# Optimization experiments

Hardware: AMD Instinct MI355X
Metric: run time of the kernel (lower is better)

The kernel has to match this reference:

```python
import jax, jax.numpy as jnp
import numpy as np

B, L, H = 32, 2048, 512
EPS = 1e-6


def setup_inputs() -> dict:
    key = jax.random.key(0)
    k1, k2 = jax.random.split(key)
    hidden = jax.random.normal(k1, (B, L, H), dtype=jnp.float32)
    # nn.Linear(H, H): weight [H, H], bias [H]; use kaiming-uniform-like scale
    bound = 1.0 / np.sqrt(H)
    W = jax.random.uniform(k2, (H, H), dtype=jnp.float32, minval=-bound, maxval=bound)
    b = jnp.zeros((H,), dtype=jnp.float32)
    return {"hidden": hidden, "W": W, "b": b}


def reference(hidden, W, b):
    Bn, Ln, Hn = hidden.shape

    def step(M, k):
        # k: [B, H]; key == value == hidden[:, t, :]
        v_pred = jnp.einsum("bij,bj->bi", M, k)               # M @ k
        denom = jnp.sum(k * k, axis=-1, keepdims=True) + EPS   # [B, 1]
        delta_v = k - v_pred / denom                           # v - v_pred/denom (v == k)
        M = M + jnp.einsum("bi,bj->bij", delta_v, k)           # outer-product update
        return M, None

    M0 = jnp.zeros((Bn, Hn, Hn), dtype=hidden.dtype)
    xs = jnp.swapaxes(hidden[:, :-1, :], 0, 1)  # [L-1, B, H]
    M, _ = jax.lax.scan(step, M0, xs)

    query = hidden[:, -1, :]                                   # [B, H]
    context = jnp.einsum("bij,bj->bi", M, query)               # [B, H]
    return context @ W.T + b                                   # read_proj
```

## Files before the change

kernel.cpp:

```cpp
#include <hip/hip_runtime.h>
#include <hip/hip_fp16.h>

#define B_  32
#define L_  2048
#define H_  512
#define T_  2047
#define CA  32
#define NC  64
#define EPSF 1e-6f

template <int CTRL>
__device__ __forceinline__ float dpp_shift_add(float x) {
  int t = __builtin_amdgcn_update_dpp(0, __float_as_int(x), CTRL, 0xf, 0xf, true);
  return x + __int_as_float(t);
}
__device__ __forceinline__ float wave_reduce_lane63(float x) {
  x = dpp_shift_add<0x111>(x);
  x = dpp_shift_add<0x112>(x);
  x = dpp_shift_add<0x114>(x);
  x = dpp_shift_add<0x118>(x);
  x = dpp_shift_add<0x142>(x);
  x = dpp_shift_add<0x143>(x);
  return x;
}
__device__ __forceinline__ float rdlane(float v, int l) {
  return __int_as_float(__builtin_amdgcn_readlane(__float_as_int(v), l));
}

__device__ __forceinline__ void load_lds16(const float* g, float* l) {
  __builtin_amdgcn_global_load_lds(
      (const __attribute__((address_space(1))) unsigned int*)(g),
      (__attribute__((address_space(3))) unsigned int*)(l), 16, 0, 0);
}
__device__ __forceinline__ void load_lds16h(const unsigned short* g, unsigned short* l) {
  __builtin_amdgcn_global_load_lds(
      (const __attribute__((address_space(1))) unsigned int*)(g),
      (__attribute__((address_space(3))) unsigned int*)(l), 16, 0, 0);
}

__global__ __launch_bounds__(256) void
deltarule_gram(const float* __restrict__ hidden,
               float* __restrict__ tmT, float* __restrict__ dvec,
               unsigned short* __restrict__ Kh,
               unsigned short* __restrict__ KhT) {
  const int cb = blockIdx.x, b = blockIdx.y;
  const int tid = threadIdx.x, lane = tid & 63, wv = tid >> 6;
  __shared__ __align__(16) float Kc[CA * H_];
  __shared__ float G[CA * 33];

  const float* kb = hidden + ((size_t)b * L_ + (size_t)cb * CA) * H_;
#pragma unroll
  for (int u = 0; u < 16; ++u) {
    const int off = (u * 4 + wv) * 256;
    load_lds16(kb + off + 4 * lane, &Kc[off]);
  }
  __asm__ volatile("s_waitcnt vmcnt(0)" ::: "memory");
  __syncthreads();
  if (cb == NC - 1) {
    if (tid < 128) *(float4*)&Kc[31 * H_ + 4 * tid] = make_float4(0.f, 0.f, 0.f, 0.f);
    __syncthreads();
  }

  if (Kh) {
    unsigned int* dst = (unsigned int*)(Kh + ((size_t)b * L_ + (size_t)cb * CA) * H_);
#pragma unroll
    for (int u = 0; u < 32; ++u) {
      const int i = u * 256 + tid;
      float2 v = *(const float2*)&Kc[2 * i];
      __half2 h2 = __floats2half2_rn(v.x, v.y);
      dst[i] = *(const unsigned int*)&h2;
      *(float2*)&Kc[2 * i] = __half22float2(h2);
    }
    __syncthreads();
  }
  if (KhT) {
    unsigned short* base = KhT + ((size_t)b * NC + cb) * (4 * H_ * 8);
#pragma unroll
    for (int r = 0; r < 2; ++r) {
      const int hh = r * 256 + tid;
#pragma unroll
      for (int g = 0; g < 4; ++g) {
        __half2 h2[4];
#pragma unroll
        for (int e = 0; e < 4; ++e) {
          float a  = Kc[(8 * g + 2 * e) * H_ + hh];
          float b2 = Kc[(8 * g + 2 * e + 1) * H_ + hh];
          h2[e] = __floats2half2_rn(a, b2);
        }
        *(uint4*)(base + (size_t)g * (H_ * 8) + (size_t)hh * 8) = *(const uint4*)h2;
      }
    }
  }

  float kr[8][8];
#pragma unroll
  for (int i = 0; i < 8; ++i) {
    const int r = 8 * wv + i;
    *(float4*)&kr[i][0] = *(const float4*)&Kc[r * H_ + 4 * lane];
    *(float4*)&kr[i][4] = *(const float4*)&Kc[r * H_ + 256 + 4 * lane];
  }
  float g[8] = {0.f, 0.f, 0.f, 0.f, 0.f, 0.f, 0.f, 0.f};
  for (int j = 8 * wv; j < CA; ++j) {
    float kj[8];
    *(float4*)&kj[0] = *(const float4*)&Kc[j * H_ + 4 * lane];
    *(float4*)&kj[4] = *(const float4*)&Kc[j * H_ + 256 + 4 * lane];
#pragma unroll
    for (int i = 0; i < 8; ++i) {
      float p = kr[i][0] * kj[0];
#pragma unroll
      for (int u = 1; u < 8; ++u) p = fmaf(kr[i][u], kj[u], p);
      p = wave_reduce_lane63(p);
      float s = rdlane(p, 63);
      g[i] = (lane == j) ? s : g[i];
    }
  }
  if (lane < CA) {
#pragma unroll
    for (int i = 0; i < 8; ++i) G[(8 * wv + i) * 33 + lane] = g[i];
  }
  __syncthreads();

  if (wv == 0) {
    const int j = lane & 31;
    float X[CA];
#pragma unroll
    for (int t = CA - 1; t >= 0; --t) {
      float inner = 0.f;
#pragma unroll
      for (int s = t + 1; s < CA; ++s) inner = fmaf(G[t * 33 + s], X[s], inner);
      X[t] = (((j == t) ? 1.f : 0.f) - inner) / (G[t * 33 + t] + EPSF);
    }
    if (lane < CA) {
      const size_t base = ((size_t)b * NC + cb) * (CA * CA);
#pragma unroll
      for (int u = 0; u < 8; ++u)
        *(float4*)&tmT[base + j * CA + 4 * u] =
            make_float4(X[4 * u], X[4 * u + 1], X[4 * u + 2], X[4 * u + 3]);
      dvec[((size_t)b * NC + cb) * CA + lane] = G[j * 33 + j] + EPSF;
    }
  }
}

__global__ __launch_bounds__(512) void
deltarule_scan_v3(const float* __restrict__ hidden,
                  const unsigned short* __restrict__ Kh,
                  const unsigned short* __restrict__ KhT,
                  const float* __restrict__ Wm, const float* __restrict__ bias,
                  const float* __restrict__ tmT, const float* __restrict__ dvec,
                  float* __restrict__ out) {
  const int b = blockIdx.x, tid = threadIdx.x, lane = tid & 63, wv = tid >> 6;
  const int j = lane & 31;
  __shared__ __align__(16) unsigned short KT[3][16384];
  __shared__ float Part[8 * 32];
  __shared__ __align__(16) float Wsw[H_];
  __shared__ __align__(16) float Ctx[H_];

  const unsigned short* khb  = Kh  + (size_t)b * L_ * H_;
  const unsigned short* khtb = KhT + (size_t)b * NC * 16384;

  float wh = hidden[(size_t)b * L_ * H_ + (size_t)(L_ - 1) * H_ + tid];
  const int wswi = ((tid & 4) << 6) + ((tid >> 3) << 2) + (tid & 3);
  Wsw[wswi] = wh;
  float ch = 0.f;

  {
    const unsigned short* src = khtb + (size_t)(NC - 1) * 16384;
#pragma unroll
    for (int u = 0; u < 4; ++u) {
      const int off = (u * 8 + wv) * 512;
      load_lds16h(src + off + 8 * lane, &KT[(NC - 1) % 3][off]);
    }
  }
  {
    const unsigned short* src = khtb + (size_t)(NC - 2) * 16384;
#pragma unroll
    for (int u = 0; u < 4; ++u) {
      const int off = (u * 8 + wv) * 512;
      load_lds16h(src + off + 8 * lane, &KT[(NC - 2) % 3][off]);
    }
  }
  float tmRow[4], dCur;
  uint4 kr[4];
  {
    const size_t tb = (size_t)b * NC + (NC - 1);
#pragma unroll
    for (int i = 0; i < 4; ++i) tmRow[i] = tmT[tb * 1024 + (4 * wv + i) * 32 + j];
    dCur = dvec[tb * 32 + j];
#pragma unroll
    for (int i = 0; i < 4; ++i)
      kr[i] = *(const uint4*)(khb + ((size_t)(NC - 1) * CA + 4 * wv + i) * H_ + 8 * lane);
  }
  asm volatile("s_waitcnt vmcnt(0) lgkmcnt(0)\n\ts_barrier" ::: "memory");

  for (int c = NC - 1; c >= 0; --c) {
    const int bufc = c % 3;

    float tmN[4], dN = 0.f;
    uint4 kn[4];
    if (c > 0) {
      const size_t tb = (size_t)b * NC + (c - 1);
#pragma unroll
      for (int i = 0; i < 4; ++i) tmN[i] = tmT[tb * 1024 + (4 * wv + i) * 32 + j];
      dN = dvec[tb * 32 + j];
#pragma unroll
      for (int i = 0; i < 4; ++i)
        kn[i] = *(const uint4*)(khb + ((size_t)(c - 1) * CA + 4 * wv + i) * H_ + 8 * lane);
    }
    asm volatile("" ::: "memory");
    if (c >= 2) {
      const unsigned short* src = khtb + (size_t)(c - 2) * 16384;
#pragma unroll
      for (int u = 0; u < 4; ++u) {
        const int off = (u * 8 + wv) * 512;
        load_lds16h(src + off + 8 * lane, &KT[(c - 2) % 3][off]);
      }
    }
    asm volatile("" ::: "memory");

    float4 wa  = *(const float4*)&Wsw[4 * lane];
    float4 wb2 = *(const float4*)&Wsw[256 + 4 * lane];
    float ysg[4];
#pragma unroll
    for (int i = 0; i < 4; ++i) {
      float2 f0 = __half22float2(*(__half2*)&kr[i].x);
      float2 f1 = __half22float2(*(__half2*)&kr[i].y);
      float2 f2 = __half22float2(*(__half2*)&kr[i].z);
      float2 f3 = __half22float2(*(__half2*)&kr[i].w);
      float p = f0.x * wa.x;
      p = fmaf(f0.y, wa.y, p); p = fmaf(f1.x, wa.z, p); p = fmaf(f1.y, wa.w, p);
      p = fmaf(f2.x, wb2.x, p); p = fmaf(f2.y, wb2.y, p);
      p = fmaf(f3.x, wb2.z, p); p = fmaf(f3.y, wb2.w, p);
      p = wave_reduce_lane63(p);
      ysg[i] = rdlane(p, 63);
    }

    float sp = ysg[0] * tmRow[0];
    sp = fmaf(ysg[1], tmRow[1], sp);
    sp = fmaf(ysg[2], tmRow[2], sp);
    sp = fmaf(ysg[3], tmRow[3], sp);
    if (lane < 32) Part[wv * 32 + j] = sp;
    asm volatile("s_waitcnt lgkmcnt(0)\n\ts_barrier" ::: "memory");

    float sig = Part[0 * 32 + j];
#pragma unroll
    for (int w2 = 1; w2 < 8; ++w2) sig += Part[w2 * 32 + j];
    float sv = dCur * sig;

    uint4 ktreg[4];
#pragma unroll
    for (int g = 0; g < 4; ++g)
      ktreg[g] = *(const uint4*)&KT[bufc][g * 4096 + tid * 8];
    const __half* kth = (const __half*)ktreg;
#pragma unroll
    for (int t = 0; t < 32; ++t) {
      float sgv = rdlane(sig, t);
      float ssv = rdlane(sv, t);
      float kv = __half2float(kth[t]);
      wh = fmaf(-sgv, kv, wh);
      ch = fmaf(ssv, kv, ch);
    }
    Wsw[wswi] = wh;

    if (c > 0) {
      dCur = dN;
#pragma unroll
      for (int i = 0; i < 4; ++i) { tmRow[i] = tmN[i]; kr[i] = kn[i]; }
    }
    if (c >= 2) {
      asm volatile("s_waitcnt vmcnt(4) lgkmcnt(0)\n\ts_barrier" ::: "memory");
    } else {
      asm volatile("s_waitcnt vmcnt(0) lgkmcnt(0)\n\ts_barrier" ::: "memory");
    }
  }

  Ctx[tid] = ch;
  __syncthreads();
  float acc = bias[tid];
  const float* wr = Wm + (size_t)tid * H_;
#pragma unroll 8
  for (int i = 0; i < H_; i += 4) {
    float4 w4 = *(const float4*)(wr + i);
    float4 cv = *(const float4*)&Ctx[i];
    acc = fmaf(w4.x, cv.x, acc); acc = fmaf(w4.y, cv.y, acc);
    acc = fmaf(w4.z, cv.z, acc); acc = fmaf(w4.w, cv.w, acc);
  }
  out[(size_t)b * H_ + tid] = acc;
}

__global__ __launch_bounds__(512) void
deltarule_scan_f32(const float* __restrict__ hidden,
                   const float* __restrict__ Wm, const float* __restrict__ bias,
                   const float* __restrict__ tmT, const float* __restrict__ dvec,
                   float* __restrict__ out) {
  const int b = blockIdx.x, tid = threadIdx.x, lane = tid & 63, wv = tid >> 6;
  __shared__ __align__(16) float Kc[2][CA * H_];
  __shared__ float Tm[CA * 33];
  __shared__ float Dv[CA];
  __shared__ float Yv[CA];
  __shared__ float2 SigS[CA];
  __shared__ __align__(16) float Wv[H_];
  __shared__ __align__(16) float Ctx[H_];

  const float* hb = hidden + (size_t)b * L_ * H_;
  float wh = hb[(size_t)(L_ - 1) * H_ + tid];
  Wv[tid] = wh;
  float ch = 0.f;

  {
    const float* kb = hb + (size_t)(NC - 1) * CA * H_;
#pragma unroll
    for (int u = 0; u < 8; ++u) {
      const int off = (u * 8 + wv) * 256;
      load_lds16(kb + off + 4 * lane, &Kc[1][off]);
    }
    const size_t tb = (size_t)b * NC + (NC - 1);
    float2 t2 = *(const float2*)&tmT[tb * (CA * CA) + 2 * tid];
    const int e0 = 2 * tid;
    Tm[(e0 >> 5) * 33 + (e0 & 31)] = t2.x;
    Tm[((e0 + 1) >> 5) * 33 + ((e0 + 1) & 31)] = t2.y;
    if (tid < CA) Dv[tid] = dvec[tb * CA + tid];
  }
  __asm__ volatile("s_waitcnt vmcnt(0)" ::: "memory");
  __syncthreads();
  if (tid < 128) *(float4*)&Kc[1][31 * H_ + 4 * tid] = make_float4(0.f, 0.f, 0.f, 0.f);
  __syncthreads();

  for (int c = NC - 1; c >= 0; --c) {
    const int buf = c & 1;
    float2 tmN = make_float2(0.f, 0.f); float dN = 0.f;
    if (c > 0) {
      const size_t tb = (size_t)b * NC + (c - 1);
      tmN = *(const float2*)&tmT[tb * (CA * CA) + 2 * tid];
      if (tid < CA) dN = dvec[tb * CA + tid];
      const float* kb = hb + (size_t)(c - 1) * CA * H_;
#pragma unroll
      for (int u = 0; u < 8; ++u) {
        const int off = (u * 8 + wv) * 256;
        load_lds16(kb + off + 4 * lane, &Kc[buf ^ 1][off]);
      }
    }
    {
      float4 wa = *(const float4*)&Wv[4 * lane];
      float4 wb = *(const float4*)&Wv[256 + 4 * lane];
#pragma unroll
      for (int i = 0; i < 4; ++i) {
        const int r = 4 * wv + i;
        float4 ka = *(const float4*)&Kc[buf][r * H_ + 4 * lane];
        float4 kc = *(const float4*)&Kc[buf][r * H_ + 256 + 4 * lane];
        float p = ka.x * wa.x;
        p = fmaf(ka.y, wa.y, p); p = fmaf(ka.z, wa.z, p); p = fmaf(ka.w, wa.w, p);
        p = fmaf(kc.x, wb.x, p); p = fmaf(kc.y, wb.y, p);
        p = fmaf(kc.z, wb.z, p); p = fmaf(kc.w, wb.w, p);
        p = wave_reduce_lane63(p);
        if (lane == 63) Yv[r] = p;
      }
    }
    __syncthreads();
    if (wv == 0) {
      const int jj = lane & 31, hf = lane >> 5;
      float sig = 0.f;
#pragma unroll
      for (int s0 = 0; s0 < 16; ++s0) {
        const int s = hf * 16 + s0;
        sig = fmaf(Tm[s * 33 + jj], Yv[s], sig);
      }
      sig += __shfl_down(sig, 32);
      if (lane < CA) SigS[jj] = make_float2(sig, Dv[jj] * sig);
    }
    __syncthreads();
    if (c > 0) {
      const int e0 = 2 * tid;
      Tm[(e0 >> 5) * 33 + (e0 & 31)] = tmN.x;
      Tm[((e0 + 1) >> 5) * 33 + ((e0 + 1) & 31)] = tmN.y;
      if (tid < CA) Dv[tid] = dN;
    }
#pragma unroll
    for (int t = 0; t < CA; ++t) {
      float2 ss = SigS[t];
      float kvv = Kc[buf][t * H_ + tid];
      wh = fmaf(-ss.x, kvv, wh);
      ch = fmaf(ss.y, kvv, ch);
    }
    Wv[tid] = wh;
    __asm__ volatile("s_waitcnt vmcnt(0)" ::: "memory");
    __syncthreads();
  }

  Ctx[tid] = ch;
  __syncthreads();
  float acc = bias[tid];
  const float* wr = Wm + (size_t)tid * H_;
#pragma unroll 8
  for (int i = 0; i < H_; i += 4) {
    float4 w4 = *(const float4*)(wr + i);
    float4 cv = *(const float4*)&Ctx[i];
    acc = fmaf(w4.x, cv.x, acc); acc = fmaf(w4.y, cv.y, acc);
    acc = fmaf(w4.z, cv.z, acc); acc = fmaf(w4.w, cv.w, acc);
  }
  out[(size_t)b * H_ + tid] = acc;
}

extern "C" void kernel_launch(void* const* d_in, const int* in_sizes, int n_in,
                              void* d_out, int out_size, void* d_ws, size_t ws_size,
                              hipStream_t stream) {
  const float* hidden = (const float*)d_in[0];
  const float* Wm     = (const float*)d_in[1];
  const float* bias   = (const float*)d_in[2];
  float* out = (float*)d_out;

  const size_t szKh  = (size_t)B_ * L_ * H_ * sizeof(unsigned short);
  const size_t szKhT = (size_t)B_ * NC * 16384 * sizeof(unsigned short);
  const size_t szTm  = (size_t)B_ * NC * CA * CA * sizeof(float);
  const size_t szD   = (size_t)B_ * NC * CA * sizeof(float);

  dim3 gridA(NC, B_);
  if (ws_size >= szKh + szKhT + szTm + szD) {
    unsigned short* Kh  = (unsigned short*)d_ws;
    unsigned short* KhT = (unsigned short*)((char*)d_ws + szKh);
    float* tmT  = (float*)((char*)d_ws + szKh + szKhT);
    float* dvec = tmT + (size_t)B_ * NC * CA * CA;
    deltarule_gram<<<gridA, 256, 0, stream>>>(hidden, tmT, dvec, Kh, KhT);
    deltarule_scan_v3<<<B_, 512, 0, stream>>>(hidden, Kh, KhT, Wm, bias, tmT, dvec, out);
  } else {
    float* tmT  = (float*)d_ws;
    float* dvec = tmT + (size_t)B_ * NC * CA * CA;
    deltarule_gram<<<gridA, 256, 0, stream>>>(hidden, tmT, dvec, nullptr, nullptr);
    deltarule_scan_f32<<<B_, 512, 0, stream>>>(hidden, Wm, bias, tmT, dvec, out);
  }
}
```

Before: 380.7 us.

## Double chunk size to 64 with MFMA Gram and block-triangular inverse

Chunk length goes from 32 to 64, which halves the number of serial chunk steps in the scan kernel. The Gram matrix is now computed with fp16 MFMA 32x32x16 instructions. The 64x64 triangular inverse is built from two 32x32 back-substitutions plus a block off-diagonal product. The transposed fp16 key copy and the fp32 fallback path are dropped, and the scan now reads keys straight from a double-buffered LDS copy. The aim is to cut per-chunk sync and latency overhead on the sequential path, at the cost of more work per step and double the LDS per buffer.

```diff
diff --git a/kernel.cpp b/kernel.cpp
--- a/kernel.cpp
+++ b/kernel.cpp
@@ -4,10 +4,12 @@
 #define B_  32
 #define L_  2048
 #define H_  512
-#define T_  2047
-#define CA  32
-#define NC  64
+#define CA  64
+#define NC  32
 #define EPSF 1e-6f
+
+typedef _Float16 f16x8 __attribute__((ext_vector_type(8)));
+typedef float f32x16 __attribute__((ext_vector_type(16)));
 
 template <int CTRL>
 __device__ __forceinline__ float dpp_shift_add(float x) {
@@ -26,12 +28,6 @@
 __device__ __forceinline__ float rdlane(float v, int l) {
   return __int_as_float(__builtin_amdgcn_readlane(__float_as_int(v), l));
 }
-
-__device__ __forceinline__ void load_lds16(const float* g, float* l) {
-  __builtin_amdgcn_global_load_lds(
-      (const __attribute__((address_space(1))) unsigned int*)(g),
-      (__attribute__((address_space(3))) unsigned int*)(l), 16, 0, 0);
-}
 __device__ __forceinline__ void load_lds16h(const unsigned short* g, unsigned short* l) {
   __builtin_amdgcn_global_load_lds(
       (const __attribute__((address_space(1))) unsigned int*)(g),
@@ -39,193 +35,205 @@
 }
 
 __global__ __launch_bounds__(256) void
-deltarule_gram(const float* __restrict__ hidden,
-               float* __restrict__ tmT, float* __restrict__ dvec,
-               unsigned short* __restrict__ Kh,
-               unsigned short* __restrict__ KhT) {
+deltarule_gram64(const float* __restrict__ hidden,
+                 unsigned short* __restrict__ Kh,
+                 float* __restrict__ tmT, float* __restrict__ dvec) {
   const int cb = blockIdx.x, b = blockIdx.y;
   const int tid = threadIdx.x, lane = tid & 63, wv = tid >> 6;
-  __shared__ __align__(16) float Kc[CA * H_];
-  __shared__ float G[CA * 33];
-
-  const float* kb = hidden + ((size_t)b * L_ + (size_t)cb * CA) * H_;
+  __shared__ __align__(16) unsigned short Kf[CA * H_];
+  __shared__ __align__(16) float G[CA * CA];
+
+  const int c0 = cb * CA;
+  const float* src = hidden + ((size_t)b * L_ + c0) * H_;
+  unsigned short* kout = Kh + ((size_t)b * L_ + c0) * H_;
+  const bool lastc = (cb == NC - 1);
+
 #pragma unroll
   for (int u = 0; u < 16; ++u) {
-    const int off = (u * 4 + wv) * 256;
-    load_lds16(kb + off + 4 * lane, &Kc[off]);
-  }
-  __asm__ volatile("s_waitcnt vmcnt(0)" ::: "memory");
-  __syncthreads();
-  if (cb == NC - 1) {
-    if (tid < 128) *(float4*)&Kc[31 * H_ + 4 * tid] = make_float4(0.f, 0.f, 0.f, 0.f);
-    __syncthreads();
-  }
-
-  if (Kh) {
-    unsigned int* dst = (unsigned int*)(Kh + ((size_t)b * L_ + (size_t)cb * CA) * H_);
-#pragma unroll
-    for (int u = 0; u < 32; ++u) {
-      const int i = u * 256 + tid;
-      float2 v = *(const float2*)&Kc[2 * i];
-      __half2 h2 = __floats2half2_rn(v.x, v.y);
-      dst[i] = *(const unsigned int*)&h2;
-      *(float2*)&Kc[2 * i] = __half22float2(h2);
-    }
-    __syncthreads();
-  }
-  if (KhT) {
-    unsigned short* base = KhT + ((size_t)b * NC + cb) * (4 * H_ * 8);
-#pragma unroll
-    for (int r = 0; r < 2; ++r) {
-      const int hh = r * 256 + tid;
-#pragma unroll
-      for (int g = 0; g < 4; ++g) {
-        __half2 h2[4];
-#pragma unroll
-        for (int e = 0; e < 4; ++e) {
-          float a  = Kc[(8 * g + 2 * e) * H_ + hh];
-          float b2 = Kc[(8 * g + 2 * e + 1) * H_ + hh];
-          h2[e] = __floats2half2_rn(a, b2);
-        }
-        *(uint4*)(base + (size_t)g * (H_ * 8) + (size_t)hh * 8) = *(const uint4*)h2;
-      }
-    }
-  }
-
-  float kr[8][8];
-#pragma unroll
-  for (int i = 0; i < 8; ++i) {
-    const int r = 8 * wv + i;
-    *(float4*)&kr[i][0] = *(const float4*)&Kc[r * H_ + 4 * lane];
-    *(float4*)&kr[i][4] = *(const float4*)&Kc[r * H_ + 256 + 4 * lane];
-  }
-  float g[8] = {0.f, 0.f, 0.f, 0.f, 0.f, 0.f, 0.f, 0.f};
-  for (int j = 8 * wv; j < CA; ++j) {
-    float kj[8];
-    *(float4*)&kj[0] = *(const float4*)&Kc[j * H_ + 4 * lane];
-    *(float4*)&kj[4] = *(const float4*)&Kc[j * H_ + 256 + 4 * lane];
-#pragma unroll
-    for (int i = 0; i < 8; ++i) {
-      float p = kr[i][0] * kj[0];
-#pragma unroll
-      for (int u = 1; u < 8; ++u) p = fmaf(kr[i][u], kj[u], p);
-      p = wave_reduce_lane63(p);
-      float s = rdlane(p, 63);
-      g[i] = (lane == j) ? s : g[i];
-    }
-  }
-  if (lane < CA) {
-#pragma unroll
-    for (int i = 0; i < 8; ++i) G[(8 * wv + i) * 33 + lane] = g[i];
-  }
+    const int f8 = u * 256 + tid;
+    const int row = f8 >> 6;
+    const int colf = (f8 & 63) * 8;
+    float4 va = *(const float4*)(src + row * H_ + colf);
+    float4 vb = *(const float4*)(src + row * H_ + colf + 4);
+    if (lastc && row == CA - 1) {
+      va = make_float4(0.f, 0.f, 0.f, 0.f);
+      vb = make_float4(0.f, 0.f, 0.f, 0.f);
+    }
+    __half2 h0 = __floats2half2_rn(va.x, va.y);
+    __half2 h1 = __floats2half2_rn(va.z, va.w);
+    __half2 h2 = __floats2half2_rn(vb.x, vb.y);
+    __half2 h3 = __floats2half2_rn(vb.z, vb.w);
+    uint4 pk = make_uint4(*(unsigned int*)&h0, *(unsigned int*)&h1,
+                          *(unsigned int*)&h2, *(unsigned int*)&h3);
+    *(uint4*)&Kf[((colf >> 3) * CA + row) * 8] = pk;
+    *(uint4*)(kout + row * H_ + colf) = pk;
+  }
+  __syncthreads();
+
+  if (wv < 3) {
+    const int ta = (wv == 2) ? 1 : 0;
+    const int tb = (wv == 0) ? 0 : 1;
+    const int mrow = 32 * ta + (lane & 31);
+    const int nrow = 32 * tb + (lane & 31);
+    const int khi = lane >> 5;
+    f32x16 acc;
+#pragma unroll
+    for (int r = 0; r < 16; ++r) acc[r] = 0.f;
+#pragma unroll
+    for (int kk = 0; kk < 32; ++kk) {
+      const int k8 = 2 * kk + khi;
+      const f16x8 av = *(const f16x8*)&Kf[(k8 * CA + mrow) * 8];
+      const f16x8 bv = *(const f16x8*)&Kf[(k8 * CA + nrow) * 8];
+      acc = __builtin_amdgcn_mfma_f32_32x32x16_f16(av, bv, acc, 0, 0, 0);
+    }
+#pragma unroll
+    for (int r = 0; r < 16; ++r) {
+      const int row32 = (r & 3) + 8 * (r >> 2) + 4 * khi;
+      G[(32 * ta + row32) * CA + 32 * tb + (lane & 31)] = acc[r];
+    }
+  }
+  __syncthreads();
+
+  if (tid < CA) dvec[((size_t)b * NC + cb) * CA + tid] = G[tid * CA + tid] + EPSF;
   __syncthreads();
 
   if (wv == 0) {
     const int j = lane & 31;
-    float X[CA];
-#pragma unroll
-    for (int t = CA - 1; t >= 0; --t) {
-      float inner = 0.f;
-#pragma unroll
-      for (int s = t + 1; s < CA; ++s) inner = fmaf(G[t * 33 + s], X[s], inner);
-      X[t] = (((j == t) ? 1.f : 0.f) - inner) / (G[t * 33 + t] + EPSF);
-    }
-    if (lane < CA) {
-      const size_t base = ((size_t)b * NC + cb) * (CA * CA);
-#pragma unroll
-      for (int u = 0; u < 8; ++u)
-        *(float4*)&tmT[base + j * CA + 4 * u] =
-            make_float4(X[4 * u], X[4 * u + 1], X[4 * u + 2], X[4 * u + 3]);
-      dvec[((size_t)b * NC + cb) * CA + lane] = G[j * 33 + j] + EPSF;
-    }
+    float X[32];
+#pragma unroll
+    for (int t = 31; t >= 0; --t) {
+      float i0 = 0.f, i1 = 0.f;
+#pragma unroll
+      for (int s = t + 1; s < 32; s += 2) i0 = fmaf(G[t * CA + s], X[s], i0);
+#pragma unroll
+      for (int s = t + 2; s < 32; s += 2) i1 = fmaf(G[t * CA + s], X[s], i1);
+      X[t] = (((j == t) ? 1.f : 0.f) - (i0 + i1)) / (G[t * CA + t] + EPSF);
+    }
+    if (lane < 32) {
+#pragma unroll
+      for (int t = 0; t < 32; ++t) G[t * CA + j] = X[t];
+    }
+  } else if (wv == 1) {
+    const int j = lane & 31;
+    float X[32];
+#pragma unroll
+    for (int t = 31; t >= 0; --t) {
+      float i0 = 0.f, i1 = 0.f;
+#pragma unroll
+      for (int s = t + 1; s < 32; s += 2) i0 = fmaf(G[(32 + t) * CA + 32 + s], X[s], i0);
+#pragma unroll
+      for (int s = t + 2; s < 32; s += 2) i1 = fmaf(G[(32 + t) * CA + 32 + s], X[s], i1);
+      X[t] = (((j == t) ? 1.f : 0.f) - (i0 + i1)) / (G[(32 + t) * CA + 32 + t] + EPSF);
+    }
+    if (lane < 32) {
+#pragma unroll
+      for (int t = 0; t < 32; ++t) G[(32 + t) * CA + 32 + j] = X[t];
+    }
+  }
+  __syncthreads();
+
+  const int zr = tid >> 3;
+  const int zc = (tid & 7) * 4;
+  float4 zf = make_float4(0.f, 0.f, 0.f, 0.f);
+#pragma unroll
+  for (int s = 0; s < 32; ++s) {
+    const float u = G[zr * CA + 32 + s];
+    const float4 xv = *(const float4*)&G[(32 + s) * CA + 32 + zc];
+    zf.x = fmaf(u, xv.x, zf.x); zf.y = fmaf(u, xv.y, zf.y);
+    zf.z = fmaf(u, xv.z, zf.z); zf.w = fmaf(u, xv.w, zf.w);
+  }
+  __syncthreads();
+  *(float4*)&G[zr * CA + 32 + zc] = zf;
+  __syncthreads();
+  float4 yf = make_float4(0.f, 0.f, 0.f, 0.f);
+#pragma unroll
+  for (int s = 0; s < 32; ++s) {
+    const float u = G[zr * CA + s];
+    const float4 zv = *(const float4*)&G[s * CA + 32 + zc];
+    yf.x = fmaf(u, zv.x, yf.x); yf.y = fmaf(u, zv.y, yf.y);
+    yf.z = fmaf(u, zv.z, yf.z); yf.w = fmaf(u, zv.w, yf.w);
+  }
+  __syncthreads();
+  *(float4*)&G[zr * CA + 32 + zc] = make_float4(-yf.x, -yf.y, -yf.z, -yf.w);
+  __syncthreads();
+
+  float* tout = tmT + ((size_t)b * NC + cb) * (CA * CA);
+#pragma unroll
+  for (int v = 0; v < 4; ++v) {
+    const int f4 = v * 256 + tid;
+    const int s = f4 >> 4;
+    const int j4 = (f4 & 15) * 4;
+    float4 val;
+    if (s >= 32 && j4 < 32) val = make_float4(0.f, 0.f, 0.f, 0.f);
+    else                    val = *(const float4*)&G[s * CA + j4];
+    *(float4*)(tout + s * CA + j4) = val;
   }
 }
 
 __global__ __launch_bounds__(512) void
-deltarule_scan_v3(const float* __restrict__ hidden,
-                  const unsigned short* __restrict__ Kh,
-                  const unsigned short* __restrict__ KhT,
-                  const float* __restrict__ Wm, const float* __restrict__ bias,
-                  const float* __restrict__ tmT, const float* __restrict__ dvec,
-                  float* __restrict__ out) {
+deltarule_scan64(const float* __restrict__ hidden,
+                 const unsigned short* __restrict__ Kh,
+                 const float* __restrict__ Wm, const float* __restrict__ bias,
+                 const float* __restrict__ tmT, const float* __restrict__ dvec,
+                 float* __restrict__ out) {
   const int b = blockIdx.x, tid = threadIdx.x, lane = tid & 63, wv = tid >> 6;
-  const int j = lane & 31;
-  __shared__ __align__(16) unsigned short KT[3][16384];
-  __shared__ float Part[8 * 32];
-  __shared__ __align__(16) float Wsw[H_];
+  __shared__ __align__(16) unsigned short KT[2][CA * H_];
+  __shared__ float Part[8 * CA];
+  __shared__ __align__(16) float Wv[H_];
   __shared__ __align__(16) float Ctx[H_];
 
-  const unsigned short* khb  = Kh  + (size_t)b * L_ * H_;
-  const unsigned short* khtb = KhT + (size_t)b * NC * 16384;
-
-  float wh = hidden[(size_t)b * L_ * H_ + (size_t)(L_ - 1) * H_ + tid];
-  const int wswi = ((tid & 4) << 6) + ((tid >> 3) << 2) + (tid & 3);
-  Wsw[wswi] = wh;
+  const unsigned short* khb = Kh + (size_t)b * L_ * H_;
+  const float* tmb = tmT + (size_t)b * NC * (CA * CA);
+  const float* dvb = dvec + (size_t)b * NC * CA;
+
+  float wh = hidden[((size_t)b * L_ + (L_ - 1)) * H_ + tid];
+  Wv[tid] = wh;
   float ch = 0.f;
 
   {
-    const unsigned short* src = khtb + (size_t)(NC - 1) * 16384;
-#pragma unroll
-    for (int u = 0; u < 4; ++u) {
+    const unsigned short* s0 = khb + (size_t)(NC - 1) * CA * H_;
+#pragma unroll
+    for (int u = 0; u < 8; ++u) {
       const int off = (u * 8 + wv) * 512;
-      load_lds16h(src + off + 8 * lane, &KT[(NC - 1) % 3][off]);
-    }
-  }
+      load_lds16h(s0 + off + 8 * lane, &KT[(NC - 1) & 1][off]);
+    }
+  }
+  float4 tA, tB; float dCur;
   {
-    const unsigned short* src = khtb + (size_t)(NC - 2) * 16384;
-#pragma unroll
-    for (int u = 0; u < 4; ++u) {
-      const int off = (u * 8 + wv) * 512;
-      load_lds16h(src + off + 8 * lane, &KT[(NC - 2) % 3][off]);
-    }
-  }
-  float tmRow[4], dCur;
-  uint4 kr[4];
-  {
-    const size_t tb = (size_t)b * NC + (NC - 1);
-#pragma unroll
-    for (int i = 0; i < 4; ++i) tmRow[i] = tmT[tb * 1024 + (4 * wv + i) * 32 + j];
-    dCur = dvec[tb * 32 + j];
-#pragma unroll
-    for (int i = 0; i < 4; ++i)
-      kr[i] = *(const uint4*)(khb + ((size_t)(NC - 1) * CA + 4 * wv + i) * H_ + 8 * lane);
+    const float* tp = tmb + (size_t)(NC - 1) * (CA * CA) + lane * CA + 8 * wv;
+    tA = *(const float4*)tp;
+    tB = *(const float4*)(tp + 4);
+    dCur = dvb[(NC - 1) * CA + lane];
   }
   asm volatile("s_waitcnt vmcnt(0) lgkmcnt(0)\n\ts_barrier" ::: "memory");
 
   for (int c = NC - 1; c >= 0; --c) {
-    const int bufc = c % 3;
-
-    float tmN[4], dN = 0.f;
-    uint4 kn[4];
+    const int buf = c & 1;
+
+    float4 nA, nB; float dN = 0.f;
     if (c > 0) {
-      const size_t tb = (size_t)b * NC + (c - 1);
-#pragma unroll
-      for (int i = 0; i < 4; ++i) tmN[i] = tmT[tb * 1024 + (4 * wv + i) * 32 + j];
-      dN = dvec[tb * 32 + j];
-#pragma unroll
-      for (int i = 0; i < 4; ++i)
-        kn[i] = *(const uint4*)(khb + ((size_t)(c - 1) * CA + 4 * wv + i) * H_ + 8 * lane);
-    }
-    asm volatile("" ::: "memory");
-    if (c >= 2) {
-      const unsigned short* src = khtb + (size_t)(c - 2) * 16384;
-#pragma unroll
-      for (int u = 0; u < 4; ++u) {
+      const float* tp = tmb + (size_t)(c - 1) * (CA * CA) + lane * CA + 8 * wv;
+      nA = *(const float4*)tp;
+      nB = *(const float4*)(tp + 4);
+      dN = dvb[(c - 1) * CA + lane];
+      const unsigned short* s1 = khb + (size_t)(c - 1) * CA * H_;
+#pragma unroll
+      for (int u = 0; u < 8; ++u) {
         const int off = (u * 8 + wv) * 512;
-        load_lds16h(src + off + 8 * lane, &KT[(c - 2) % 3][off]);
+        load_lds16h(s1 + off + 8 * lane, &KT[buf ^ 1][off]);
       }
     }
-    asm volatile("" ::: "memory");
-
-    float4 wa  = *(const float4*)&Wsw[4 * lane];
-    float4 wb2 = *(const float4*)&Wsw[256 + 4 * lane];
-    float ysg[4];
-#pragma unroll
-    for (int i = 0; i < 4; ++i) {
-      float2 f0 = __half22float2(*(__half2*)&kr[i].x);
-      float2 f1 = __half22float2(*(__half2*)&kr[i].y);
-      float2 f2 = __half22float2(*(__half2*)&kr[i].z);
-      float2 f3 = __half22float2(*(__half2*)&kr[i].w);
+
+    const float4 wa  = *(const float4*)&Wv[8 * lane];
+    const float4 wb2 = *(const float4*)&Wv[8 * lane + 4];
+    float ysg[8];
+#pragma unroll
+    for (int i = 0; i < 8; ++i) {
+      const uint4 kr = *(const uint4*)&KT[buf][(8 * wv + i) * H_ + 8 * lane];
+      const float2 f0 = __half22float2(*(const __half2*)&kr.x);
+      const float2 f1 = __half22float2(*(const __half2*)&kr.y);
+      const float2 f2 = __half22float2(*(const __half2*)&kr.z);
+      const float2 f3 = __half22float2(*(const __half2*)&kr.w);
       float p = f0.x * wa.x;
       p = fmaf(f0.y, wa.y, p); p = fmaf(f1.x, wa.z, p); p = fmaf(f1.y, wa.w, p);
       p = fmaf(f2.x, wb2.x, p); p = fmaf(f2.y, wb2.y, p);
@@ -234,43 +242,35 @@
       ysg[i] = rdlane(p, 63);
     }
 
-    float sp = ysg[0] * tmRow[0];
-    sp = fmaf(ysg[1], tmRow[1], sp);
-    sp = fmaf(ysg[2], tmRow[2], sp);
-    sp = fmaf(ysg[3], tmRow[3], sp);
-    if (lane < 32) Part[wv * 32 + j] = sp;
+    float sp = ysg[0] * tA.x;
+    sp = fmaf(ysg[1], tA.y, sp); sp = fmaf(ysg[2], tA.z, sp);
+    sp = fmaf(ysg[3], tA.w, sp); sp = fmaf(ysg[4], tB.x, sp);
+    sp = fmaf(ysg[5], tB.y, sp); sp = fmaf(ysg[6], tB.z, sp);
+    sp = fmaf(ysg[7], tB.w, sp);
+    Part[wv * CA + lane] = sp;
     asm volatile("s_waitcnt lgkmcnt(0)\n\ts_barrier" ::: "memory");
 
-    float sig = Part[0 * 32 + j];
-#pragma unroll
-    for (int w2 = 1; w2 < 8; ++w2) sig += Part[w2 * 32 + j];
-    float sv = dCur * sig;
-
-    uint4 ktreg[4];
-#pragma unroll
-    for (int g = 0; g < 4; ++g)
-      ktreg[g] = *(const uint4*)&KT[bufc][g * 4096 + tid * 8];
-    const __half* kth = (const __half*)ktreg;
-#pragma unroll
-    for (int t = 0; t < 32; ++t) {
-      float sgv = rdlane(sig, t);
-      float ssv = rdlane(sv, t);
-      float kv = __half2float(kth[t]);
-      wh = fmaf(-sgv, kv, wh);
-      ch = fmaf(ssv, kv, ch);
-    }
-    Wsw[wswi] = wh;
-
-    if (c > 0) {
-      dCur = dN;
-#pragma unroll
-      for (int i = 0; i < 4; ++i) { tmRow[i] = tmN[i]; kr[i] = kn[i]; }
-    }
-    if (c >= 2) {
-      asm volatile("s_waitcnt vmcnt(4) lgkmcnt(0)\n\ts_barrier" ::: "memory");
-    } else {
-      asm volatile("s_waitcnt vmcnt(0) lgkmcnt(0)\n\ts_barrier" ::: "memory");
-    }
+    float sig = Part[lane];
+#pragma unroll
+    for (int w2 = 1; w2 < 8; ++w2) sig += Part[w2 * CA + lane];
+    const float sv = dCur * sig;
+
+    float dw0 = 0.f, dw1 = 0.f, dc0 = 0.f, dc1 = 0.f;
+#pragma unroll
+    for (int t = 0; t < CA; t += 2) {
+      const float kv0 = __half2float(*(const __half*)&KT[buf][t * H_ + tid]);
+      const float kv1 = __half2float(*(const __half*)&KT[buf][(t + 1) * H_ + tid]);
+      dw0 = fmaf(rdlane(sig, t), kv0, dw0);
+      dc0 = fmaf(rdlane(sv, t), kv0, dc0);
+      dw1 = fmaf(rdlane(sig, t + 1), kv1, dw1);
+      dc1 = fmaf(rdlane(sv, t + 1), kv1, dc1);
+    }
+    wh -= dw0 + dw1;
+    ch += dc0 + dc1;
+    Wv[tid] = wh;
+
+    if (c > 0) { dCur = dN; tA = nA; tB = nB; }
+    asm volatile("s_waitcnt vmcnt(0) lgkmcnt(0)\n\ts_barrier" ::: "memory");
   }
 
   Ctx[tid] = ch;
@@ -279,121 +279,8 @@
   const float* wr = Wm + (size_t)tid * H_;
 #pragma unroll 8
   for (int i = 0; i < H_; i += 4) {
-    float4 w4 = *(const float4*)(wr + i);
-    float4 cv = *(const float4*)&Ctx[i];
-    acc = fmaf(w4.x, cv.x, acc); acc = fmaf(w4.y, cv.y, acc);
-    acc = fmaf(w4.z, cv.z, acc); acc = fmaf(w4.w, cv.w, acc);
-  }
-  out[(size_t)b * H_ + tid] = acc;
-}
-
-__global__ __launch_bounds__(512) void
-deltarule_scan_f32(const float* __restrict__ hidden,
-                   const float* __restrict__ Wm, const float* __restrict__ bias,
-                   const float* __restrict__ tmT, const float* __restrict__ dvec,
-                   float* __restrict__ out) {
-  const int b = blockIdx.x, tid = threadIdx.x, lane = tid & 63, wv = tid >> 6;
-  __shared__ __align__(16) float Kc[2][CA * H_];
-  __shared__ float Tm[CA * 33];
-  __shared__ float Dv[CA];
-  __shared__ float Yv[CA];
-  __shared__ float2 SigS[CA];
-  __shared__ __align__(16) float Wv[H_];
-  __shared__ __align__(16) float Ctx[H_];
-
-  const float* hb = hidden + (size_t)b * L_ * H_;
-  float wh = hb[(size_t)(L_ - 1) * H_ + tid];
-  Wv[tid] = wh;
-  float ch = 0.f;
-
-  {
-    const float* kb = hb + (size_t)(NC - 1) * CA * H_;
-#pragma unroll
-    for (int u = 0; u < 8; ++u) {
-      const int off = (u * 8 + wv) * 256;
-      load_lds16(kb + off + 4 * lane, &Kc[1][off]);
-    }
-    const size_t tb = (size_t)b * NC + (NC - 1);
-    float2 t2 = *(const float2*)&tmT[tb * (CA * CA) + 2 * tid];
-    const int e0 = 2 * tid;
-    Tm[(e0 >> 5) * 33 + (e0 & 31)] = t2.x;
-    Tm[((e0 + 1) >> 5) * 33 + ((e0 + 1) & 31)] = t2.y;
-    if (tid < CA) Dv[tid] = dvec[tb * CA + tid];
-  }
-  __asm__ volatile("s_waitcnt vmcnt(0)" ::: "memory");
-  __syncthreads();
-  if (tid < 128) *(float4*)&Kc[1][31 * H_ + 4 * tid] = make_float4(0.f, 0.f, 0.f, 0.f);
-  __syncthreads();
-
-  for (int c = NC - 1; c >= 0; --c) {
-    const int buf = c & 1;
-    float2 tmN = make_float2(0.f, 0.f); float dN = 0.f;
-    if (c > 0) {
-      const size_t tb = (size_t)b * NC + (c - 1);
-      tmN = *(const float2*)&tmT[tb * (CA * CA) + 2 * tid];
-      if (tid < CA) dN = dvec[tb * CA + tid];
-      const float* kb = hb + (size_t)(c - 1) * CA * H_;
-#pragma unroll
-      for (int u = 0; u < 8; ++u) {
-        const int off = (u * 8 + wv) * 256;
-        load_lds16(kb + off + 4 * lane, &Kc[buf ^ 1][off]);
-      }
-    }
-    {
-      float4 wa = *(const float4*)&Wv[4 * lane];
-      float4 wb = *(const float4*)&Wv[256 + 4 * lane];
-#pragma unroll
-      for (int i = 0; i < 4; ++i) {
-        const int r = 4 * wv + i;
-        float4 ka = *(const float4*)&Kc[buf][r * H_ + 4 * lane];
-        float4 kc = *(const float4*)&Kc[buf][r * H_ + 256 + 4 * lane];
-        float p = ka.x * wa.x;
-        p = fmaf(ka.y, wa.y, p); p = fmaf(ka.z, wa.z, p); p = fmaf(ka.w, wa.w, p);
-        p = fmaf(kc.x, wb.x, p); p = fmaf(kc.y, wb.y, p);
-        p = fmaf(kc.z, wb.z, p); p = fmaf(kc.w, wb.w, p);
-        p = wave_reduce_lane63(p);
-        if (lane == 63) Yv[r] = p;
-      }
-    }
-    __syncthreads();
-    if (wv == 0) {
-      const int jj = lane & 31, hf = lane >> 5;
-      float sig = 0.f;
-#pragma unroll
-      for (int s0 = 0; s0 < 16; ++s0) {
-        const int s = hf * 16 + s0;
-        sig = fmaf(Tm[s * 33 + jj], Yv[s], sig);
-      }
-      sig += __shfl_down(sig, 32);
-      if (lane < CA) SigS[jj] = make_float2(sig, Dv[jj] * sig);
-    }
-    __syncthreads();
-    if (c > 0) {
-      const int e0 = 2 * tid;
-      Tm[(e0 >> 5) * 33 + (e0 & 31)] = tmN.x;
-      Tm[((e0 + 1) >> 5) * 33 + ((e0 + 1) & 31)] = tmN.y;
-      if (tid < CA) Dv[tid] = dN;
-    }
-#pragma unroll
-    for (int t = 0; t < CA; ++t) {
-      float2 ss = SigS[t];
-      float kvv = Kc[buf][t * H_ + tid];
-      wh = fmaf(-ss.x, kvv, wh);
-      ch = fmaf(ss.y, kvv, ch);
-    }
-    Wv[tid] = wh;
-    __asm__ volatile("s_waitcnt vmcnt(0)" ::: "memory");
-    __syncthreads();
-  }
-
-  Ctx[tid] = ch;
-  __syncthreads();
-  float acc = bias[tid];
-  const float* wr = Wm + (size_t)tid * H_;
-#pragma unroll 8
-  for (int i = 0; i < H_; i += 4) {
-    float4 w4 = *(const float4*)(wr + i);
-    float4 cv = *(const float4*)&Ctx[i];
+    const float4 w4 = *(const float4*)(wr + i);
+    const float4 cv = *(const float4*)&Ctx[i];
     acc = fmaf(w4.x, cv.x, acc); acc = fmaf(w4.y, cv.y, acc);
     acc = fmaf(w4.z, cv.z, acc); acc = fmaf(w4.w, cv.w, acc);
   }
@@ -403,28 +290,17 @@
 extern "C" void kernel_launch(void* const* d_in, const int* in_sizes, int n_in,
                               void* d_out, int out_size, void* d_ws, size_t ws_size,
                               hipStream_t stream) {
+  (void)in_sizes; (void)n_in; (void)out_size; (void)ws_size;
   const float* hidden = (const float*)d_in[0];
   const float* Wm     = (const float*)d_in[1];
   const float* bias   = (const float*)d_in[2];
   float* out = (float*)d_out;
 
-  const size_t szKh  = (size_t)B_ * L_ * H_ * sizeof(unsigned short);
-  const size_t szKhT = (size_t)B_ * NC * 16384 * sizeof(unsigned short);
-  const size_t szTm  = (size_t)B_ * NC * CA * CA * sizeof(float);
-  const size_t szD   = (size_t)B_ * NC * CA * sizeof(float);
-
-  dim3 gridA(NC, B_);
-  if (ws_size >= szKh + szKhT + szTm + szD) {
-    unsigned short* Kh  = (unsigned short*)d_ws;
-    unsigned short* KhT = (unsigned short*)((char*)d_ws + szKh);
-    float* tmT  = (float*)((char*)d_ws + szKh + szKhT);
-    float* dvec = tmT + (size_t)B_ * NC * CA * CA;
-    deltarule_gram<<<gridA, 256, 0, stream>>>(hidden, tmT, dvec, Kh, KhT);
-    deltarule_scan_v3<<<B_, 512, 0, stream>>>(hidden, Kh, KhT, Wm, bias, tmT, dvec, out);
-  } else {
-    float* tmT  = (float*)d_ws;
-    float* dvec = tmT + (size_t)B_ * NC * CA * CA;
-    deltarule_gram<<<gridA, 256, 0, stream>>>(hidden, tmT, dvec, nullptr, nullptr);
-    deltarule_scan_f32<<<B_, 512, 0, stream>>>(hidden, Wm, bias, tmT, dvec, out);
-  }
-}
+  const size_t szKh = (size_t)B_ * L_ * H_ * sizeof(unsigned short);
+  unsigned short* Kh = (unsigned short*)d_ws;
+  float* tmT  = (float*)((char*)d_ws + szKh);
+  float* dvec = tmT + (size_t)B_ * NC * CA * CA;
+
+  deltarule_gram64<<<dim3(NC, B_), 256, 0, stream>>>(hidden, Kh, tmT, dvec);
+  deltarule_scan64<<<B_, 512, 0, stream>>>(hidden, Kh, Wm, bias, tmT, dvec, out);
+}
```

New measurement: 344.6 us. 1.1x faster.
